# Kernel optimization log

Hardware: AMD Instinct MI355X
Metric: run time of the kernel (lower is better)

The kernel has to match this reference:

```python
import jax, jax.numpy as jnp
import numpy as np
import math

DROPOUT_P = 0.1

def setup_inputs() -> dict:
    key = jax.random.key(0)
    k1, k2, k3 = jax.random.split(key, 3)
    B, Lq, Lk, D = 8, 2048, 2048, 128
    x1 = jax.random.normal(k1, (B, Lq, D), dtype=jnp.float32)
    x2 = jax.random.normal(k2, (B, Lk, D), dtype=jnp.float32)
    qm = jnp.zeros((1, Lq, Lk), dtype=jnp.float32)  # additive attention mask
    u = jax.random.uniform(k3, (B, Lq, Lk), dtype=jnp.float32)  # dropout uniforms
    return {"x1": x1, "x2": x2, "qm": qm, "u": u}

def reference(x1, x2, qm, u):
    # scaled dot-product attention with additive mask + inverted dropout
    scale = 1.0 / math.sqrt(x1.shape[-1])
    qk = jnp.einsum('bqd,bkd->bqk', x1, x2) * scale + qm  # [B, Lq, Lk]
    attn = jax.nn.softmax(qk, axis=-1)
    keep = (u >= DROPOUT_P).astype(attn.dtype) / (1.0 - DROPOUT_P)
    attn = attn * keep
    out = jnp.einsum('bqk,bkd->bqd', attn, x2)  # [B, Lq, D]
    return out
```

## Files before the change

### kernel.cpp

```cpp
#include <hip/hip_runtime.h>
#include <hip/hip_bf16.h>
#include <stdint.h>

#define LQ 2048
#define LK 2048
#define DH 128
#define BQ 64
#define KB 128
#define NT (LK / KB)
#define KROW 136
#define LOG2E 1.44269504088896340736f
#define QSCALE 0.088388347648318447f

typedef __attribute__((ext_vector_type(8)))  short bf16x8;
typedef __attribute__((ext_vector_type(16))) float f32x16;
typedef __attribute__((ext_vector_type(4)))  float f32x4;

union FragAB { uint32_t u[4]; bf16x8 v; };

__device__ __forceinline__ uint32_t pack2_bf16(float lo, float hi) {
  union { __hip_bfloat16 b; uint16_t u; } a, c;
  a.b = __float2bfloat16(lo);
  c.b = __float2bfloat16(hi);
  return (uint32_t)a.u | ((uint32_t)c.u << 16);
}

__global__ __launch_bounds__(256)
void qmt_kernel(const float* __restrict__ qm, uint16_t* __restrict__ qmt2) {
  const int kc = threadIdx.x & 63;
  const int q  = blockIdx.x * 4 + (threadIdx.x >> 6);
  f32x4 r[8];
  const float* src = qm + (size_t)q * 2048 + kc * 32;
#pragma unroll
  for (int c = 0; c < 8; ++c) r[c] = *(const f32x4*)(src + c * 4);
#pragma unroll
  for (int h = 0; h < 2; ++h) {
    uint32_t w[8];
#pragma unroll
    for (int i = 0; i < 8; ++i) {
      const int gi0 = 2 * i, gi1 = 2 * i + 1;
      const float v0 = r[h + (gi0 >> 2) * 2][gi0 & 3] * LOG2E;
      const float v1 = r[h + (gi1 >> 2) * 2][gi1 & 3] * LOG2E;
      w[i] = pack2_bf16(v0, v1);
    }
    uint16_t* dst = qmt2 + ((size_t)(kc * 2 + h) * 2048 + q) * 16;
    uint4 lo = {w[0], w[1], w[2], w[3]};
    uint4 hi = {w[4], w[5], w[6], w[7]};
    *(uint4*)dst = lo;
    *(uint4*)(dst + 8) = hi;
  }
}

__device__ __forceinline__ void stage_writes(uint16_t* Kb, uint16_t* Vb,
                                             const f32x4* st, int sbi, int sbj) {
#pragma unroll
  for (int j = 0; j < 2; ++j) {
    const int rowb = 4 * (sbi + 16 * j);
#pragma unroll
    for (int r = 0; r < 4; ++r) {
      f32x4 v = st[j * 4 + r];
      uint64_t pk = (uint64_t)pack2_bf16(v.x, v.y) |
                    ((uint64_t)pack2_bf16(v.z, v.w) << 32);
      *(uint64_t*)(Kb + (size_t)(rowb + r) * KROW + 4 * sbj) = pk;
    }
#pragma unroll
    for (int c = 0; c < 4; ++c) {
      uint64_t pv = (uint64_t)pack2_bf16(st[j * 4 + 0][c], st[j * 4 + 1][c]) |
                    ((uint64_t)pack2_bf16(st[j * 4 + 2][c], st[j * 4 + 3][c]) << 32);
      const size_t off = ((size_t)(4 * sbj + c) * KROW + rowb) ^ (size_t)((sbj & 7) << 3);
      *(uint64_t*)(Vb + off) = pv;
    }
  }
}

__global__ __launch_bounds__(512, 2)
void fattn_kernel(const float* __restrict__ x1, const float* __restrict__ x2,
                  const float* __restrict__ uu,
                  const uint16_t* __restrict__ qmt2,
                  float* __restrict__ out)
{
  __shared__ uint16_t ldsK[2][128 * KROW];
  __shared__ uint16_t ldsV[2][128 * KROW];

  const int tid  = threadIdx.x;
  const int wv   = tid >> 6;
  const int lane = tid & 63;
  const int ln   = lane & 31;
  const int h    = lane >> 5;
  const int qsub = wv & 1;
  const int ks   = wv >> 1;

  const int b    = blockIdx.x & 7;
  const int qblk = blockIdx.x >> 3;
  const int qbase = qblk * BQ + qsub * 32;
  const int qrow  = qbase + ln;

  FragAB qf[8];
  {
    const float* qp = x1 + ((size_t)(b * LQ + qrow)) * DH + h * 8;
    const float qs = QSCALE * LOG2E;
#pragma unroll
    for (int dc = 0; dc < 8; ++dc) {
      f32x4 a = *(const f32x4*)(qp + dc * 16);
      f32x4 c = *(const f32x4*)(qp + dc * 16 + 4);
      qf[dc].u[0] = pack2_bf16(a.x * qs, a.y * qs);
      qf[dc].u[1] = pack2_bf16(a.z * qs, a.w * qs);
      qf[dc].u[2] = pack2_bf16(c.x * qs, c.y * qs);
      qf[dc].u[3] = pack2_bf16(c.z * qs, c.w * qs);
    }
  }

  const int sbi = tid >> 5;
  const int sbj = tid & 31;
  const float* x2base = x2 + (size_t)b * LK * DH + sbj * 4;
  const float* ub = uu + ((size_t)(b * LQ + qbase + h)) * LK + ks * 32 + ln;
  const int vxor = ((ln >> 2) & 7) << 3;

  f32x4 st[8];
#pragma unroll
  for (int j = 0; j < 2; ++j)
#pragma unroll
    for (int r = 0; r < 4; ++r)
      st[j * 4 + r] = *(const f32x4*)(x2base + (size_t)(4 * (sbi + 16 * j) + r) * DH);

  float ucur[16];
#pragma unroll
  for (int i = 0; i < 16; ++i)
    ucur[i] = __builtin_nontemporal_load(ub + (size_t)(2 * i) * LK);

  uint4 qc0, qc1;
  {
    const uint16_t* qp16 = qmt2 + (((size_t)(0 * 4 + ks) * 2 + h) * 2048 + qrow) * 16;
    qc0 = *(const uint4*)qp16;
    qc1 = *(const uint4*)(qp16 + 8);
  }

  stage_writes(ldsK[0], ldsV[0], st, sbi, sbj);
  __syncthreads();

  float m_run = -1e30f, l_run = 0.f;
  f32x16 acco[4];
#pragma unroll
  for (int d2 = 0; d2 < 4; ++d2)
#pragma unroll
    for (int i = 0; i < 16; ++i) acco[d2][i] = 0.f;

  for (int t = 0; t < NT; ++t) {
    const int cb = t & 1;
    const uint16_t* Kb = ldsK[cb];
    const uint16_t* Vb = ldsV[cb];
    const int kb = t * KB;

    float unxt[16]; uint4 qn0, qn1;
    if (t + 1 < NT) {
#pragma unroll
      for (int j = 0; j < 2; ++j)
#pragma unroll
        for (int r = 0; r < 4; ++r)
          st[j * 4 + r] = *(const f32x4*)(x2base + (size_t)(kb + KB + 4 * (sbi + 16 * j) + r) * DH);
#pragma unroll
      for (int i = 0; i < 16; ++i)
        unxt[i] = __builtin_nontemporal_load(ub + (size_t)(kb + KB) + (size_t)(2 * i) * LK);
      const uint16_t* qp16 = qmt2 + (((size_t)((t + 1) * 4 + ks) * 2 + h) * 2048 + qrow) * 16;
      qn0 = *(const uint4*)qp16;
      qn1 = *(const uint4*)(qp16 + 8);
    }

    f32x16 sacc;
#pragma unroll
    for (int i = 0; i < 16; ++i) sacc[i] = 0.f;
    const uint16_t* Krow = Kb + (size_t)(ks * 32 + ln) * KROW + h * 8;
    __builtin_amdgcn_s_setprio(1);
#pragma unroll
    for (int dc = 0; dc < 8; ++dc) {
      bf16x8 af = *(const bf16x8*)(Krow + dc * 16);
      sacc = __builtin_amdgcn_mfma_f32_32x32x16_bf16(af, qf[dc].v, sacc, 0, 0, 0);
    }
    __builtin_amdgcn_s_setprio(0);

#define ADDQM(W, I) { sacc[I] += __uint_as_float((W) << 16); \
                      sacc[I + 1] += __uint_as_float((W) & 0xffff0000u); }
    ADDQM(qc0.x, 0)  ADDQM(qc0.y, 2)  ADDQM(qc0.z, 4)  ADDQM(qc0.w, 6)
    ADDQM(qc1.x, 8)  ADDQM(qc1.y, 10) ADDQM(qc1.z, 12) ADDQM(qc1.w, 14)
#undef ADDQM

    float pm = sacc[0];
#pragma unroll
    for (int i = 1; i < 16; ++i) pm = fmaxf(pm, sacc[i]);
    pm = fmaxf(pm, __shfl_xor(pm, 32));
    const float mnew = fmaxf(m_run, pm);
    const float resc = __builtin_amdgcn_exp2f(m_run - mnew);
    m_run = mnew;
    float rs = 0.f;
#pragma unroll
    for (int i = 0; i < 16; ++i) {
      sacc[i] = __builtin_amdgcn_exp2f(sacc[i] - mnew);
      rs += sacc[i];
    }
    rs += __shfl_xor(rs, 32);
    l_run = l_run * resc + rs;

    uint32_t M = 0;
#pragma unroll
    for (int i = 0; i < 16; ++i) {
      unsigned long long bi = __ballot(ucur[i] >= 0.1f);
      uint32_t sel = (ln & 1) ? (uint32_t)(bi >> 32) : (uint32_t)bi;
      M = ((ln >> 1) == i) ? sel : M;
    }
#pragma unroll
    for (int g = 0; g < 4; ++g)
#pragma unroll
      for (int j2 = 0; j2 < 4; ++j2) {
        const uint32_t keep = (M >> (h * 4 + g * 8 + j2)) & 1u;
        sacc[g * 4 + j2] = keep ? sacc[g * 4 + j2] : 0.f;
      }

    uint32_t pr[4][2], sw[4][2];
#pragma unroll
    for (int g = 0; g < 4; ++g) {
      pr[g][0] = pack2_bf16(sacc[4 * g + 0], sacc[4 * g + 1]);
      pr[g][1] = pack2_bf16(sacc[4 * g + 2], sacc[4 * g + 3]);
      sw[g][0] = __shfl_xor(pr[g][0], 32);
      sw[g][1] = __shfl_xor(pr[g][1], 32);
    }
    FragAB bfr[2];
#pragma unroll
    for (int c = 0; c < 2; ++c) {
      bfr[c].u[0] = h ? sw[2 * c + 1][0] : pr[2 * c][0];
      bfr[c].u[1] = h ? sw[2 * c + 1][1] : pr[2 * c][1];
      bfr[c].u[2] = h ? pr[2 * c + 1][0] : sw[2 * c][0];
      bfr[c].u[3] = h ? pr[2 * c + 1][1] : sw[2 * c][1];
    }

#pragma unroll
    for (int d2 = 0; d2 < 4; ++d2)
#pragma unroll
      for (int i = 0; i < 16; ++i) acco[d2][i] *= resc;

    __builtin_amdgcn_s_setprio(1);
#pragma unroll
    for (int d2 = 0; d2 < 4; ++d2) {
#pragma unroll
      for (int c = 0; c < 2; ++c) {
        const size_t voff = (((size_t)(d2 * 32 + ln)) * KROW + ks * 32 + h * 8 + c * 16) ^ (size_t)vxor;
        bf16x8 av = *(const bf16x8*)(Vb + voff);
        acco[d2] = __builtin_amdgcn_mfma_f32_32x32x16_bf16(av, bfr[c].v, acco[d2], 0, 0, 0);
      }
    }
    __builtin_amdgcn_s_setprio(0);

    if (t + 1 < NT) {
      stage_writes(ldsK[cb ^ 1], ldsV[cb ^ 1], st, sbi, sbj);
#pragma unroll
      for (int i = 0; i < 16; ++i) ucur[i] = unxt[i];
      qc0 = qn0; qc1 = qn1;
    }
    __syncthreads();
  }

  float* scr = (wv < 4) ? ((float*)ldsK + (size_t)wv * 4224)
                        : ((float*)ldsV + (size_t)(wv - 4) * 4224);
  scr[lane]      = m_run;
  scr[64 + lane] = l_run;
#pragma unroll
  for (int d2 = 0; d2 < 4; ++d2)
#pragma unroll
    for (int g = 0; g < 4; ++g) {
      f32x4 vv;
#pragma unroll
      for (int j2 = 0; j2 < 4; ++j2) vv[j2] = acco[d2][g * 4 + j2];
      *(f32x4*)(scr + 128 + (size_t)(d2 * 4 + g) * 256 + lane * 4) = vv;
    }
  __syncthreads();

  if (wv < 2) {
    const float* rg[4];
#pragma unroll
    for (int s2 = 0; s2 < 4; ++s2) {
      const int r = qsub + 2 * s2;
      rg[s2] = (r < 4) ? ((const float*)ldsK + (size_t)r * 4224)
                       : ((const float*)ldsV + (size_t)(r - 4) * 4224);
    }
    const float ms0 = rg[0][lane], ms1 = rg[1][lane], ms2 = rg[2][lane], ms3 = rg[3][lane];
    const float ls0 = rg[0][64 + lane], ls1 = rg[1][64 + lane];
    const float ls2 = rg[2][64 + lane], ls3 = rg[3][64 + lane];
    const float mM = fmaxf(fmaxf(ms0, ms1), fmaxf(ms2, ms3));
    const float e0 = __builtin_amdgcn_exp2f(ms0 - mM);
    const float e1 = __builtin_amdgcn_exp2f(ms1 - mM);
    const float e2 = __builtin_amdgcn_exp2f(ms2 - mM);
    const float e3 = __builtin_amdgcn_exp2f(ms3 - mM);
    const float lM = e0 * ls0 + e1 * ls1 + e2 * ls2 + e3 * ls3;
    const float inv = (1.0f / 0.9f) / lM;
    float* op = out + ((size_t)(b * LQ + qblk * BQ + qsub * 32 + lane % 32)) * DH;
    (void)op;
    const int lq = lane & 31;
    float* op2 = out + ((size_t)(b * LQ + qblk * BQ + qsub * 32 + lq)) * DH;
    const int hh = lane >> 5;
#pragma unroll
    for (int d2 = 0; d2 < 4; ++d2)
#pragma unroll
      for (int g = 0; g < 4; ++g) {
        const size_t off = 128 + (size_t)(d2 * 4 + g) * 256 + lane * 4;
        f32x4 a4 = e0 * *(const f32x4*)(rg[0] + off)
                 + e1 * *(const f32x4*)(rg[1] + off)
                 + e2 * *(const f32x4*)(rg[2] + off)
                 + e3 * *(const f32x4*)(rg[3] + off);
        a4 = a4 * inv;
        *(f32x4*)(op2 + d2 * 32 + 8 * g + 4 * hh) = a4;
      }
  }
}

extern "C" void kernel_launch(void* const* d_in, const int* in_sizes, int n_in,
                              void* d_out, int out_size, void* d_ws, size_t ws_size,
                              hipStream_t stream) {
  (void)in_sizes; (void)n_in; (void)out_size; (void)ws_size;
  const float* x1 = (const float*)d_in[0];
  const float* x2 = (const float*)d_in[1];
  const float* qm = (const float*)d_in[2];
  const float* u  = (const float*)d_in[3];
  float* out = (float*)d_out;

  uint16_t* qmt2 = (uint16_t*)d_ws;

  qmt_kernel<<<dim3(512), dim3(256), 0, stream>>>(qm, qmt2);
  fattn_kernel<<<dim3(256), dim3(512), 0, stream>>>(x1, x2, u, qmt2, out);
}
```

Measured before the change: 245.1 us.

## Pre-convert K/V to bf16 and stream tiles into LDS with direct loads

A new prep kernel converts x2 to bf16 once, storing K row-major and V transposed in workspace. The attention kernel then fills LDS with global_load_lds DMA loads instead of loading fp32 into registers, packing and writing to LDS. The block shrinks to 256 threads and 32 query rows over 512 blocks, with a single LDS buffer. This removes the per-tile conversion work and register staging, but gives up double-buffered overlap: each tile load is waited on before compute, and the prep kernel adds an extra pass.

```diff
diff --git a/kernel.cpp b/kernel.cpp
--- a/kernel.cpp
+++ b/kernel.cpp
@@ -5,16 +5,19 @@
 #define LQ 2048
 #define LK 2048
 #define DH 128
-#define BQ 64
+#define BQ 32
 #define KB 128
 #define NT (LK / KB)
-#define KROW 136
+#define KROWE 136
 #define LOG2E 1.44269504088896340736f
 #define QSCALE 0.088388347648318447f
 
 typedef __attribute__((ext_vector_type(8)))  short bf16x8;
 typedef __attribute__((ext_vector_type(16))) float f32x16;
 typedef __attribute__((ext_vector_type(4)))  float f32x4;
+
+typedef __attribute__((address_space(1))) const void glob_cv;
+typedef __attribute__((address_space(3))) void lds_v;
 
 union FragAB { uint32_t u[4]; bf16x8 v; };
 
@@ -23,6 +26,44 @@
   a.b = __float2bfloat16(lo);
   c.b = __float2bfloat16(hi);
   return (uint32_t)a.u | ((uint32_t)c.u << 16);
+}
+
+__global__ __launch_bounds__(256)
+void prep_kernel(const float* __restrict__ x2, uint16_t* __restrict__ Kp,
+                 uint16_t* __restrict__ Vp) {
+  __shared__ uint16_t tl[128][130];
+  const int b = blockIdx.x & 7, tile = blockIdx.x >> 3;
+  const int t = threadIdx.x;
+  const int row0 = t >> 1, half = t & 1;
+
+  const float* src = x2 + ((size_t)(b * 2048 + tile * 128 + row0)) * 128 + half * 64;
+  uint32_t wbuf[32];
+#pragma unroll
+  for (int i = 0; i < 16; ++i) {
+    f32x4 v = *(const f32x4*)(src + i * 4);
+    wbuf[2 * i]     = pack2_bf16(v.x, v.y);
+    wbuf[2 * i + 1] = pack2_bf16(v.z, v.w);
+  }
+  uint16_t* kdst = Kp + ((size_t)(b * 2048 + tile * 128 + row0)) * 128 + half * 64;
+#pragma unroll
+  for (int i = 0; i < 8; ++i)
+    *(uint4*)(kdst + i * 8) = *(const uint4*)&wbuf[i * 4];
+#pragma unroll
+  for (int i = 0; i < 32; ++i)
+    *(uint32_t*)&tl[row0][half * 64 + 2 * i] = wbuf[i];
+  __syncthreads();
+
+  const int d = t >> 1, halfk = t & 1;
+  uint32_t vw[32];
+#pragma unroll
+  for (int i = 0; i < 32; ++i) {
+    const int k = halfk * 64 + 2 * i;
+    vw[i] = (uint32_t)tl[k][d] | ((uint32_t)tl[k + 1][d] << 16);
+  }
+  uint16_t* vdst = Vp + ((size_t)(b * 128 + d)) * 2048 + tile * 128 + halfk * 64;
+#pragma unroll
+  for (int i = 0; i < 8; ++i)
+    *(uint4*)(vdst + i * 8) = *(const uint4*)&vw[i * 4];
 }
 
 __global__ __launch_bounds__(256)
@@ -51,48 +92,27 @@
   }
 }
 
-__device__ __forceinline__ void stage_writes(uint16_t* Kb, uint16_t* Vb,
-                                             const f32x4* st, int sbi, int sbj) {
-#pragma unroll
-  for (int j = 0; j < 2; ++j) {
-    const int rowb = 4 * (sbi + 16 * j);
-#pragma unroll
-    for (int r = 0; r < 4; ++r) {
-      f32x4 v = st[j * 4 + r];
-      uint64_t pk = (uint64_t)pack2_bf16(v.x, v.y) |
-                    ((uint64_t)pack2_bf16(v.z, v.w) << 32);
-      *(uint64_t*)(Kb + (size_t)(rowb + r) * KROW + 4 * sbj) = pk;
-    }
-#pragma unroll
-    for (int c = 0; c < 4; ++c) {
-      uint64_t pv = (uint64_t)pack2_bf16(st[j * 4 + 0][c], st[j * 4 + 1][c]) |
-                    ((uint64_t)pack2_bf16(st[j * 4 + 2][c], st[j * 4 + 3][c]) << 32);
-      const size_t off = ((size_t)(4 * sbj + c) * KROW + rowb) ^ (size_t)((sbj & 7) << 3);
-      *(uint64_t*)(Vb + off) = pv;
-    }
-  }
-}
-
-__global__ __launch_bounds__(512, 2)
-void fattn_kernel(const float* __restrict__ x1, const float* __restrict__ x2,
+__global__ __launch_bounds__(256, 2)
+void fattn_kernel(const float* __restrict__ x1,
+                  const uint16_t* __restrict__ Kp,
+                  const uint16_t* __restrict__ Vp,
                   const float* __restrict__ uu,
                   const uint16_t* __restrict__ qmt2,
                   float* __restrict__ out)
 {
-  __shared__ uint16_t ldsK[2][128 * KROW];
-  __shared__ uint16_t ldsV[2][128 * KROW];
+  __shared__ char lds[69632];
+  uint16_t* lds16 = (uint16_t*)lds;
 
   const int tid  = threadIdx.x;
   const int wv   = tid >> 6;
   const int lane = tid & 63;
   const int ln   = lane & 31;
   const int h    = lane >> 5;
-  const int qsub = wv & 1;
-  const int ks   = wv >> 1;
-
-  const int b    = blockIdx.x & 7;
-  const int qblk = blockIdx.x >> 3;
-  const int qbase = qblk * BQ + qsub * 32;
+  const int ks   = wv;
+
+  const int b     = blockIdx.x & 7;
+  const int qblk  = blockIdx.x >> 3;
+  const int qbase = qblk * BQ;
   const int qrow  = qbase + ln;
 
   FragAB qf[8];
@@ -110,18 +130,34 @@
     }
   }
 
-  const int sbi = tid >> 5;
-  const int sbj = tid & 31;
-  const float* x2base = x2 + (size_t)b * LK * DH + sbj * 4;
+  int koffs[9], voffs[9];
+#pragma unroll
+  for (int jj = 0; jj < 9; ++jj) {
+    const int j = jj * 4 + wv;
+    if (j < 34) {
+      const int G = j * 64 + lane;
+      const int row = (G * 61681) >> 20;
+      const int s0  = G - row * 17;
+      const int s   = (s0 < 16) ? s0 : 0;
+      koffs[jj] = row * 256  + s * 16;
+      voffs[jj] = row * 4096 + s * 16;
+    } else { koffs[jj] = 0; voffs[jj] = 0; }
+  }
+  const char* Kpb = (const char*)(Kp + (size_t)b * 2048 * 128);
+  const char* Vpb = (const char*)(Vp + (size_t)b * 128 * 2048);
+
   const float* ub = uu + ((size_t)(b * LQ + qbase + h)) * LK + ks * 32 + ln;
-  const int vxor = ((ln >> 2) & 7) << 3;
-
-  f32x4 st[8];
-#pragma unroll
-  for (int j = 0; j < 2; ++j)
-#pragma unroll
-    for (int r = 0; r < 4; ++r)
-      st[j * 4 + r] = *(const f32x4*)(x2base + (size_t)(4 * (sbi + 16 * j) + r) * DH);
+
+#pragma unroll
+  for (int jj = 0; jj < 9; ++jj) {
+    const int j = jj * 4 + wv;
+    if (j < 34) {
+      __builtin_amdgcn_global_load_lds((glob_cv*)(Kpb + koffs[jj]),
+                                       (lds_v*)(lds + j * 1024), 16, 0, 0);
+      __builtin_amdgcn_global_load_lds((glob_cv*)(Vpb + voffs[jj]),
+                                       (lds_v*)(lds + 34816 + j * 1024), 16, 0, 0);
+    }
+  }
 
   float ucur[16];
 #pragma unroll
@@ -130,12 +166,10 @@
 
   uint4 qc0, qc1;
   {
-    const uint16_t* qp16 = qmt2 + (((size_t)(0 * 4 + ks) * 2 + h) * 2048 + qrow) * 16;
+    const uint16_t* qp16 = qmt2 + (((size_t)ks * 2 + h) * 2048 + qrow) * 16;
     qc0 = *(const uint4*)qp16;
     qc1 = *(const uint4*)(qp16 + 8);
   }
-
-  stage_writes(ldsK[0], ldsV[0], st, sbi, sbj);
   __syncthreads();
 
   float m_run = -1e30f, l_run = 0.f;
@@ -146,21 +180,11 @@
     for (int i = 0; i < 16; ++i) acco[d2][i] = 0.f;
 
   for (int t = 0; t < NT; ++t) {
-    const int cb = t & 1;
-    const uint16_t* Kb = ldsK[cb];
-    const uint16_t* Vb = ldsV[cb];
-    const int kb = t * KB;
-
     float unxt[16]; uint4 qn0, qn1;
     if (t + 1 < NT) {
 #pragma unroll
-      for (int j = 0; j < 2; ++j)
-#pragma unroll
-        for (int r = 0; r < 4; ++r)
-          st[j * 4 + r] = *(const f32x4*)(x2base + (size_t)(kb + KB + 4 * (sbi + 16 * j) + r) * DH);
-#pragma unroll
       for (int i = 0; i < 16; ++i)
-        unxt[i] = __builtin_nontemporal_load(ub + (size_t)(kb + KB) + (size_t)(2 * i) * LK);
+        unxt[i] = __builtin_nontemporal_load(ub + (size_t)((t + 1) * KB) + (size_t)(2 * i) * LK);
       const uint16_t* qp16 = qmt2 + (((size_t)((t + 1) * 4 + ks) * 2 + h) * 2048 + qrow) * 16;
       qn0 = *(const uint4*)qp16;
       qn1 = *(const uint4*)(qp16 + 8);
@@ -169,7 +193,7 @@
     f32x16 sacc;
 #pragma unroll
     for (int i = 0; i < 16; ++i) sacc[i] = 0.f;
-    const uint16_t* Krow = Kb + (size_t)(ks * 32 + ln) * KROW + h * 8;
+    const uint16_t* Krow = lds16 + (size_t)(ks * 32 + ln) * KROWE + h * 8;
     __builtin_amdgcn_s_setprio(1);
 #pragma unroll
     for (int dc = 0; dc < 8; ++dc) {
@@ -240,26 +264,37 @@
     __builtin_amdgcn_s_setprio(1);
 #pragma unroll
     for (int d2 = 0; d2 < 4; ++d2) {
+      const uint16_t* Vrow = lds16 + 17408 + (size_t)(d2 * 32 + ln) * KROWE + ks * 32 + h * 8;
 #pragma unroll
       for (int c = 0; c < 2; ++c) {
-        const size_t voff = (((size_t)(d2 * 32 + ln)) * KROW + ks * 32 + h * 8 + c * 16) ^ (size_t)vxor;
-        bf16x8 av = *(const bf16x8*)(Vb + voff);
+        bf16x8 av = *(const bf16x8*)(Vrow + c * 16);
         acco[d2] = __builtin_amdgcn_mfma_f32_32x32x16_bf16(av, bfr[c].v, acco[d2], 0, 0, 0);
       }
     }
     __builtin_amdgcn_s_setprio(0);
 
+    __syncthreads();
     if (t + 1 < NT) {
-      stage_writes(ldsK[cb ^ 1], ldsV[cb ^ 1], st, sbi, sbj);
+      const char* kp = Kpb + (size_t)(t + 1) * 32768;
+      const char* vp = Vpb + (size_t)(t + 1) * 256;
+#pragma unroll
+      for (int jj = 0; jj < 9; ++jj) {
+        const int j = jj * 4 + wv;
+        if (j < 34) {
+          __builtin_amdgcn_global_load_lds((glob_cv*)(kp + koffs[jj]),
+                                           (lds_v*)(lds + j * 1024), 16, 0, 0);
+          __builtin_amdgcn_global_load_lds((glob_cv*)(vp + voffs[jj]),
+                                           (lds_v*)(lds + 34816 + j * 1024), 16, 0, 0);
+        }
+      }
 #pragma unroll
       for (int i = 0; i < 16; ++i) ucur[i] = unxt[i];
       qc0 = qn0; qc1 = qn1;
-    }
-    __syncthreads();
-  }
-
-  float* scr = (wv < 4) ? ((float*)ldsK + (size_t)wv * 4224)
-                        : ((float*)ldsV + (size_t)(wv - 4) * 4224);
+      __syncthreads();
+    }
+  }
+
+  float* scr = (float*)lds + (size_t)wv * 4224;
   scr[lane]      = m_run;
   scr[64 + lane] = l_run;
 #pragma unroll
@@ -276,11 +311,7 @@
   if (wv < 2) {
     const float* rg[4];
 #pragma unroll
-    for (int s2 = 0; s2 < 4; ++s2) {
-      const int r = qsub + 2 * s2;
-      rg[s2] = (r < 4) ? ((const float*)ldsK + (size_t)r * 4224)
-                       : ((const float*)ldsV + (size_t)(r - 4) * 4224);
-    }
+    for (int s2 = 0; s2 < 4; ++s2) rg[s2] = (const float*)lds + (size_t)s2 * 4224;
     const float ms0 = rg[0][lane], ms1 = rg[1][lane], ms2 = rg[2][lane], ms3 = rg[3][lane];
     const float ls0 = rg[0][64 + lane], ls1 = rg[1][64 + lane];
     const float ls2 = rg[2][64 + lane], ls3 = rg[3][64 + lane];
@@ -291,13 +322,10 @@
     const float e3 = __builtin_amdgcn_exp2f(ms3 - mM);
     const float lM = e0 * ls0 + e1 * ls1 + e2 * ls2 + e3 * ls3;
     const float inv = (1.0f / 0.9f) / lM;
-    float* op = out + ((size_t)(b * LQ + qblk * BQ + qsub * 32 + lane % 32)) * DH;
-    (void)op;
-    const int lq = lane & 31;
-    float* op2 = out + ((size_t)(b * LQ + qblk * BQ + qsub * 32 + lq)) * DH;
-    const int hh = lane >> 5;
-#pragma unroll
-    for (int d2 = 0; d2 < 4; ++d2)
+    float* op = out + ((size_t)(b * LQ + qbase + ln)) * DH;
+#pragma unroll
+    for (int dd = 0; dd < 2; ++dd) {
+      const int d2 = wv * 2 + dd;
 #pragma unroll
       for (int g = 0; g < 4; ++g) {
         const size_t off = 128 + (size_t)(d2 * 4 + g) * 256 + lane * 4;
@@ -306,8 +334,9 @@
                  + e2 * *(const f32x4*)(rg[2] + off)
                  + e3 * *(const f32x4*)(rg[3] + off);
         a4 = a4 * inv;
-        *(f32x4*)(op2 + d2 * 32 + 8 * g + 4 * hh) = a4;
+        *(f32x4*)(op + d2 * 32 + 8 * g + 4 * h) = a4;
       }
+    }
   }
 }
 
@@ -322,7 +351,10 @@
   float* out = (float*)d_out;
 
   uint16_t* qmt2 = (uint16_t*)d_ws;
-
+  uint16_t* Kp   = (uint16_t*)((char*)d_ws + (8u  << 20));
+  uint16_t* Vp   = (uint16_t*)((char*)d_ws + (12u << 20));
+
+  prep_kernel<<<dim3(128), dim3(256), 0, stream>>>(x2, Kp, Vp);
   qmt_kernel<<<dim3(512), dim3(256), 0, stream>>>(qm, qmt2);
-  fattn_kernel<<<dim3(256), dim3(512), 0, stream>>>(x1, x2, u, qmt2, out);
-}
+  fattn_kernel<<<dim3(512), dim3(256), 0, stream>>>(x1, Kp, Vp, u, qmt2, out);
+}
```

Measured after the change: 248.8 us. Within noise of the previous version (+1.5%).
